# Kernel tuning notes

Measured on AMD Instinct MI355X. Metric: run time of the kernel, lower is better.

## Reference

```python
import jax, jax.numpy as jnp
import numpy as np

H = 4  # num heads, hard-coded in Encoder's GAT(hidden, hidden, hidden, 4, 2)


def build_adjacency(shot_type, encode_length):
    # Faithful vectorized port of initialize_adjacency_matrix.
    B, S = shot_type.shape
    N = 2 * encode_length
    base = np.zeros((14, N, N), dtype=np.int32)
    base[13] = 1 - np.eye(N, dtype=np.int32)  # complete graph minus self-loops
    for row in range(N):
        ni = row // 2
        if row % 2 == 0:
            col = (ni + 1) * 2
            rel = 11 if ni % 2 == 0 else 12
        else:
            col = (ni + 1) * 2 + 1
            rel = 12 if ni % 2 == 0 else 11
        if col <= N - 1:
            base[rel, row, col] = 1
            base[rel, col, row] = 1
            base[13, row, col] = 0
            base[13, col, row] = 0
    adj = jnp.tile(jnp.asarray(base)[None], (B, 1, 1, 1))  # [B,14,N,N]
    steps = np.arange(S)
    even = steps % 2 == 0
    i = np.where(even, 2 * steps, 2 * steps + 1)
    j = np.where(even, 2 * (steps + 1) + 1, 2 * (steps + 1))
    b = np.broadcast_to(np.arange(B)[:, None], (B, S))
    i = np.broadcast_to(i, (B, S))
    j = np.broadcast_to(j, (B, S))
    adj = adj.at[b, shot_type, i, j].set(1)
    adj = adj.at[b, shot_type, j, i].set(1)
    adj = adj.at[b, 13, i, j].set(0)
    adj = adj.at[b, 13, j, i].set(0)
    return adj


def gat_layer(x, mask, W, att):
    # x: [B,N,in], W: [in, H*F], att: [H, 2F]; standard GAT concat-score,
    # computed as a_src.h_i + a_dst.h_j (== a^T [h_i || h_j]).
    B, N, _ = x.shape
    F = att.shape[1] // 2
    h = (x @ W).reshape(B, N, H, F).transpose(0, 2, 1, 3)       # [B,H,N,F]
    s_src = jnp.einsum('bhnf,hf->bhn', h, att[:, :F])
    s_dst = jnp.einsum('bhnf,hf->bhn', h, att[:, F:])
    scores = s_src[:, :, :, None] + s_dst[:, :, None, :]        # [B,H,N,N]
    scores = jnp.where(scores > 0, scores, 0.2 * scores)        # LeakyReLU(0.2)
    scores = jnp.where(mask[:, None], scores, -jnp.inf)
    attn = jax.nn.softmax(scores, axis=-1)                      # dropout: eval mode
    hp = jnp.einsum('bhij,bhjf->bhif', attn, h)
    return hp.transpose(0, 2, 1, 3).reshape(B, N, H * F)


def setup_inputs() -> dict:
    B, E = 32, 256
    player_num, player_dim, location_dim, hidden = 35, 32, 32, 64
    k = jax.random.split(jax.random.key(0), 16)

    def lin(key, fan_in, shape):
        return jax.random.normal(key, shape, dtype=jnp.float32) / np.sqrt(fan_in)

    return {
        'player': jax.random.randint(k[0], (B, 2), 0, player_num),
        'shot_type': jax.random.randint(k[1], (B, E - 1), 0, 11),
        'player_A_x': jax.random.uniform(k[2], (B, E), dtype=jnp.float32),
        'player_A_y': jax.random.uniform(k[3], (B, E), dtype=jnp.float32),
        'player_B_x': jax.random.uniform(k[4], (B, E), dtype=jnp.float32),
        'player_B_y': jax.random.uniform(k[5], (B, E), dtype=jnp.float32),
        'encode_length': E,
        'emb_table': jax.random.normal(k[6], (player_num, player_dim), dtype=jnp.float32),
        'Wc': lin(k[7], 2, (2, location_dim)),
        'bc': jnp.zeros((location_dim,), dtype=jnp.float32),
        'Wm': lin(k[8], player_dim + location_dim, (player_dim + location_dim, hidden)),
        'bm': jnp.zeros((hidden,), dtype=jnp.float32),
        'lin1_W': lin(k[9], hidden, (hidden, H * hidden)),
        'att1': lin(k[10], 2 * hidden, (H, 2 * hidden)),
        'lin2_W': lin(k[11], H * hidden, (H * hidden, H * hidden)),
        'att2': lin(k[12], 2 * hidden, (H, 2 * hidden)),
    }


def reference(player, shot_type, player_A_x, player_A_y, player_B_x, player_B_y,
              encode_length, emb_table, Wc, bc, Wm, bm, lin1_W, att1, lin2_W, att2):
    E = int(encode_length)
    B = player.shape[0]
    adj = build_adjacency(shot_type, E)                 # [B,14,N,N]
    mask = adj.sum(axis=1) > 0                          # union over relations [B,N,N]
    coord_A = jnp.stack([player_A_x, player_A_y], axis=-1)   # [B,E,2]
    coord_B = jnp.stack([player_B_x, player_B_y], axis=-1)
    coord = jnp.stack([coord_A, coord_B], axis=2).reshape(B, -1, 2)  # [B,2E,2]
    ct = jax.nn.relu(coord @ Wc + bc)                   # [B,2E,loc]
    p = jnp.tile(player, (1, E))                        # [B,2E]
    pe = emb_table[p]                                   # [B,2E,pdim]
    x = jnp.concatenate([ct, pe], axis=-1) @ Wm + bm    # [B,2E,hidden]
    x = jax.nn.relu(gat_layer(x, mask, lin1_W, att1))
    node_embedding = gat_layer(x, mask, lin2_W, att2)   # [B,2E,H*hidden]
    return node_embedding, adj
```

## Files before the change

kernel.cpp:

```cpp
#include <hip/hip_runtime.h>
#include <hip/hip_bf16.h>
#include <stdint.h>

static constexpr int B_  = 32;
static constexpr int E_  = 256;
static constexpr int N_  = 512;
static constexpr int C_  = 256;
static constexpr int BN  = B_ * N_;
static constexpr int NODE_ELEMS = B_ * N_ * C_;
static constexpr int ADJ_ELEMS  = B_ * 14 * N_ * N_;

#define LOG2E 1.44269504088896340736f

typedef __attribute__((ext_vector_type(8))) short v8bf;
typedef __attribute__((ext_vector_type(4))) float v4f;

__device__ __forceinline__ unsigned short f2bfbits(float f) {
  union { float f; unsigned u; } x; x.f = f;
  unsigned u = x.u;
  return (unsigned short)((u + 0x7FFFu + ((u >> 16) & 1u)) >> 16);
}

struct ConvArgs {
  const void* src[15];
  void* dst[15];
  int n[15];
  int kind[15];
};

__global__ __launch_bounds__(256) void k_conv2(ConvArgs a, const unsigned* fprobe,
                                               const unsigned* iprobe) {
  __shared__ int fk_s, ik_s;
  int t = threadIdx.x;
  if (t == 0) {
    int c_even = 0, c_lo = 0;
    for (int k = 0; k < 32; ++k) {
      unsigned w = fprobe[2 * k];
      unsigned e32 = (w >> 23) & 0xFFu;
      unsigned elo = (w >> 7) & 0xFFu;
      if (e32 >= 105u && e32 <= 135u) ++c_even;
      if (elo >= 105u && elo <= 135u) ++c_lo;
    }
    fk_s = (c_even < 16) ? 2 : ((c_lo >= 16) ? 1 : 0);
    int hi0 = 0;
    for (int k = 0; k < 32; ++k) if (iprobe[2 * k + 1] == 0u) ++hi0;
    ik_s = (hi0 >= 30) ? 1 : 0;
  }
  __syncthreads();
  int fk = fk_s, ik = ik_s;
  int arr = blockIdx.y;
  int n = a.n[arr], kind = a.kind[arr];
  for (int idx = blockIdx.x * 256 + t; idx < n; idx += gridDim.x * 256) {
    if (kind == 0) {
      float v;
      if (fk == 2) {
        v = (float)((const double*)a.src[arr])[idx];
      } else if (fk == 1) {
        unsigned short u = ((const unsigned short*)a.src[arr])[idx];
        union { unsigned u; float f; } c; c.u = (unsigned)u << 16; v = c.f;
      } else {
        v = ((const float*)a.src[arr])[idx];
      }
      ((float*)a.dst[arr])[idx] = v;
    } else {
      int v;
      if (ik == 1) v = (int)((const long long*)a.src[arr])[idx];
      else         v = ((const int*)a.src[arr])[idx];
      ((int*)a.dst[arr])[idx] = v;
    }
  }
}

__global__ __launch_bounds__(64) void k_feat2(
    const int* __restrict__ player, const float* __restrict__ Ax, const float* __restrict__ Ay,
    const float* __restrict__ Bx, const float* __restrict__ By,
    const float* __restrict__ emb, const float* __restrict__ Wc, const float* __restrict__ bc,
    const float* __restrict__ Wm, const float* __restrict__ bm, float* __restrict__ x) {
  int id = blockIdx.x * 64 + threadIdx.x;
  if (id >= BN) return;
  int b = id >> 9, n = id & 511;
  int e = n >> 1, side = n & 1;
  float cx = side ? Bx[b * E_ + e] : Ax[b * E_ + e];
  float cy = side ? By[b * E_ + e] : Ay[b * E_ + e];
  int pid = player[b * 2 + side];
  float ct[32];
  for (int k = 0; k < 32; ++k)
    ct[k] = fmaxf(fmaf(cx, Wc[k], fmaf(cy, Wc[32 + k], bc[k])), 0.f);
  for (int o = 0; o < 64; ++o) {
    float acc = bm[o];
    for (int c = 0; c < 32; ++c) acc = fmaf(ct[c], Wm[c * 64 + o], acc);
    for (int c = 0; c < 32; ++c) acc = fmaf(emb[pid * 32 + c], Wm[(32 + c) * 64 + o], acc);
    x[(size_t)id * 64 + o] = acc;
  }
}

__global__ __launch_bounds__(256) void k_gemm(
    const float* __restrict__ x, const float* __restrict__ W, float* __restrict__ h, int K) {
  __shared__ float xs[64 * 64];
  __shared__ float wt[64 * 64];
  int row0 = blockIdx.x * 64;
  int col0 = blockIdx.y * 64;
  int t = threadIdx.x;
  int tx = t & 15, ty = t >> 4;
  float acc[4][4] = {};
  for (int kt = 0; kt < K; kt += 64) {
    #pragma unroll
    for (int q = 0; q < 4; ++q) {
      int v = q * 256 + t;
      int r = v >> 4, c = (v & 15) * 4;
      *(float4*)&xs[r * 64 + c] = *(const float4*)&x[(size_t)(row0 + r) * K + kt + c];
      *(float4*)&wt[r * 64 + c] = *(const float4*)&W[(size_t)(kt + r) * C_ + col0 + c];
    }
    __syncthreads();
    #pragma unroll 4
    for (int k = 0; k < 64; ++k) {
      float xv[4];
      #pragma unroll
      for (int r = 0; r < 4; ++r) xv[r] = xs[(ty * 4 + r) * 64 + k];
      float4 wf = *(const float4*)&wt[k * 64 + tx * 4];
      #pragma unroll
      for (int r = 0; r < 4; ++r) {
        acc[r][0] = fmaf(xv[r], wf.x, acc[r][0]);
        acc[r][1] = fmaf(xv[r], wf.y, acc[r][1]);
        acc[r][2] = fmaf(xv[r], wf.z, acc[r][2]);
        acc[r][3] = fmaf(xv[r], wf.w, acc[r][3]);
      }
    }
    __syncthreads();
  }
  #pragma unroll
  for (int r = 0; r < 4; ++r) {
    int row = row0 + ty * 4 + r;
    float4 o = make_float4(acc[r][0], acc[r][1], acc[r][2], acc[r][3]);
    *(float4*)&h[(size_t)row * C_ + col0 + tx * 4] = o;
  }
}

__global__ __launch_bounds__(256) void k_ssd(
    const float* __restrict__ h, const float* __restrict__ att,
    float* __restrict__ ss, float* __restrict__ sd) {
  int t = threadIdx.x;
  int wv = t >> 6, l = t & 63;
  int row = blockIdx.x * 4 + wv;
  int b = row >> 9, n = row & 511;
  #pragma unroll
  for (int hd = 0; hd < 4; ++hd) {
    float v = h[(size_t)row * C_ + hd * 64 + l];
    float s1 = v * att[hd * 128 + l];
    float s2 = v * att[hd * 128 + 64 + l];
    #pragma unroll
    for (int d = 32; d > 0; d >>= 1) {
      s1 += __shfl_xor(s1, d, 64);
      s2 += __shfl_xor(s2, d, 64);
    }
    if (l == 0) {
      int idx = (b * 4 + hd) * N_ + n;
      ss[idx] = s1; sd[idx] = s2;
    }
  }
}

__global__ __launch_bounds__(256) void k_ml(
    const float* __restrict__ ss, const float* __restrict__ sd,
    float* __restrict__ m2, float* __restrict__ rl) {
  int t = threadIdx.x;
  int wv = t >> 6, l = t & 63;
  int row = blockIdx.x * 4 + wv;
  int bh = row >> 9, i = row & 511;
  const float* sdb = sd + (size_t)bh * N_;
  float mx = -1e30f;
  #pragma unroll
  for (int q = 0; q < 8; ++q) mx = fmaxf(mx, sdb[q * 64 + l]);
  #pragma unroll
  for (int d = 32; d > 0; d >>= 1) mx = fmaxf(mx, __shfl_xor(mx, d, 64));
  float ssi = ss[row];
  float s = ssi + mx;
  float mm2 = fmaxf(s, 0.2f * s) * LOG2E;
  float acc = 0.f;
  #pragma unroll
  for (int q = 0; q < 8; ++q) {
    int j = q * 64 + l;
    float sc = ssi + sdb[j];
    sc = fmaxf(sc, 0.2f * sc);
    float e = exp2f(fmaf(sc, LOG2E, -mm2));
    acc += (j == i) ? 0.f : e;
  }
  #pragma unroll
  for (int d = 32; d > 0; d >>= 1) acc += __shfl_xor(acc, d, 64);
  if (l == 0) { m2[row] = mm2; rl[row] = 1.f / acc; }
}

template <int RELU>
__global__ __launch_bounds__(256) void k_attn_mfma(
    const float* __restrict__ h, const float* __restrict__ ss, const float* __restrict__ sd,
    const float* __restrict__ m2, const float* __restrict__ rl, float* __restrict__ outf) {
  __shared__ unsigned short hs[64 * 72];
  __shared__ float sdl[64];
  int blk = blockIdx.x;
  int it = blk & 3, hd = (blk >> 2) & 3, b = blk >> 4;
  int i0 = it * 128;
  int bh = b * 4 + hd;
  int t = threadIdx.x;
  int w = t >> 6, l = t & 63;
  int lane16 = l & 15, quad = l >> 4;
  float ss_s[2], m2_s[2];
  #pragma unroll
  for (int s = 0; s < 2; ++s) {
    int i = i0 + w * 32 + s * 16 + lane16;
    ss_s[s] = ss[(size_t)bh * N_ + i];
    m2_s[s] = m2[(size_t)bh * N_ + i];
  }
  v4f acc[2][4] = {};
  for (int jt = 0; jt < 8; ++jt) {
    int j0 = jt * 64;
    #pragma unroll
    for (int q = 0; q < 4; ++q) {
      int v = q * 256 + t;
      int j = v >> 4, f0 = (v & 15) * 4;
      float4 hv = *(const float4*)&h[(size_t)(b * N_ + j0 + j) * C_ + hd * 64 + f0];
      hs[(f0 + 0) * 72 + j] = f2bfbits(hv.x);
      hs[(f0 + 1) * 72 + j] = f2bfbits(hv.y);
      hs[(f0 + 2) * 72 + j] = f2bfbits(hv.z);
      hs[(f0 + 3) * 72 + j] = f2bfbits(hv.w);
    }
    if (t < 64) sdl[t] = sd[(size_t)bh * N_ + j0 + t];
    __syncthreads();
    #pragma unroll
    for (int ks = 0; ks < 2; ++ks) {
      int kb = ks * 32;
      v8bf afr[2];
      #pragma unroll
      for (int s = 0; s < 2; ++s) {
        int i = i0 + w * 32 + s * 16 + lane16;
        #pragma unroll
        for (int q = 0; q < 8; ++q) {
          int j = kb + quad * 8 + q;
          float sv = ss_s[s] + sdl[j];
          float sc = fmaxf(sv, 0.2f * sv);
          float p = exp2f(fmaf(sc, LOG2E, -m2_s[s]));
          if (i == j0 + j) p = 0.f;
          afr[s][q] = (short)f2bfbits(p);
        }
      }
      #pragma unroll
      for (int fs = 0; fs < 4; ++fs) {
        v8bf bfr = *(const v8bf*)&hs[(fs * 16 + lane16) * 72 + kb + quad * 8];
        acc[0][fs] = __builtin_amdgcn_mfma_f32_16x16x32_bf16(afr[0], bfr, acc[0][fs], 0, 0, 0);
        acc[1][fs] = __builtin_amdgcn_mfma_f32_16x16x32_bf16(afr[1], bfr, acc[1][fs], 0, 0, 0);
      }
    }
    __syncthreads();
  }
  #pragma unroll
  for (int s = 0; s < 2; ++s) {
    #pragma unroll
    for (int r = 0; r < 4; ++r) {
      int i = i0 + w * 32 + s * 16 + quad * 4 + r;
      float scale = rl[(size_t)bh * N_ + i];
      #pragma unroll
      for (int fs = 0; fs < 4; ++fs) {
        int f = fs * 16 + lane16;
        float vv = acc[s][fs][r] * scale;
        if constexpr (RELU) vv = fmaxf(vv, 0.f);
        outf[(size_t)(b * N_ + i) * C_ + hd * 64 + f] = vv;
      }
    }
  }
}

__global__ __launch_bounds__(256) void k_adjf2(
    const int* __restrict__ st, float* __restrict__ adj) {
  int chunk = blockIdx.x * 256 + threadIdx.x;
  int j0 = (chunk & 127) << 2;
  int rowid = chunk >> 7;
  int i = rowid & 511;
  int plane = rowid >> 9;
  int r = plane % 14;
  int b = plane / 14;
  float vals[4];
  #pragma unroll
  for (int q = 0; q < 4; ++q) {
    int j = j0 + q;
    int d = j - i;
    int ad = d < 0 ? -d : d;
    int mn = d < 0 ? j : i;
    int m4 = mn & 3;
    float v = 0.f;
    if (r == 13) {
      bool excl = (d == 0) || (ad == 2) || (ad == 3 && m4 == 0) || (ad == 1 && m4 == 3);
      v = excl ? 0.f : 1.f;
    } else if (r == 11) {
      v = (ad == 2 && (m4 == 0 || m4 == 3)) ? 1.f : 0.f;
    } else if (r == 12) {
      v = (ad == 2 && (m4 == 1 || m4 == 2)) ? 1.f : 0.f;
    } else {
      bool sp = (ad == 3 && m4 == 0) || (ad == 1 && m4 == 3);
      if (sp) v = (st[b * 255 + (mn >> 1)] == r) ? 1.f : 0.f;
    }
    vals[q] = v;
  }
  *(float4*)&adj[(size_t)chunk * 4] = make_float4(vals[0], vals[1], vals[2], vals[3]);
}

__global__ __launch_bounds__(256) void k_adjf(
    const unsigned* __restrict__ st_raw, float* __restrict__ adj) {
  __shared__ int i64_s;
  if (threadIdx.x == 0) {
    int hi0 = 0;
    for (int k = 0; k < 32; ++k) if (st_raw[2 * k + 1] == 0u) ++hi0;
    i64_s = (hi0 >= 30) ? 1 : 0;
  }
  __syncthreads();
  int is64 = i64_s;
  int chunk = blockIdx.x * 256 + threadIdx.x;
  int j0 = (chunk & 127) << 2;
  int rowid = chunk >> 7;
  int i = rowid & 511;
  int plane = rowid >> 9;
  int r = plane % 14;
  int b = plane / 14;
  float vals[4];
  #pragma unroll
  for (int q = 0; q < 4; ++q) {
    int j = j0 + q;
    int d = j - i;
    int ad = d < 0 ? -d : d;
    int mn = d < 0 ? j : i;
    int m4 = mn & 3;
    float v = 0.f;
    if (r == 13) {
      bool excl = (d == 0) || (ad == 2) || (ad == 3 && m4 == 0) || (ad == 1 && m4 == 3);
      v = excl ? 0.f : 1.f;
    } else if (r == 11) {
      v = (ad == 2 && (m4 == 0 || m4 == 3)) ? 1.f : 0.f;
    } else if (r == 12) {
      v = (ad == 2 && (m4 == 1 || m4 == 2)) ? 1.f : 0.f;
    } else {
      bool sp = (ad == 3 && m4 == 0) || (ad == 1 && m4 == 3);
      if (sp) {
        int e = b * 255 + (mn >> 1);
        int stv = is64 ? (int)st_raw[2 * e] : (int)st_raw[e];
        v = (stv == r) ? 1.f : 0.f;
      }
    }
    vals[q] = v;
  }
  *(float4*)&adj[(size_t)chunk * 4] = make_float4(vals[0], vals[1], vals[2], vals[3]);
}

__global__ void k_sentinel(float* out, float v) {
  if (threadIdx.x == 0 && blockIdx.x == 0) out[0] = v;
}

extern "C" void kernel_launch(void* const* d_in, const int* in_sizes, int n_in,
                              void* d_out, int out_size, void* d_ws, size_t ws_size,
                              hipStream_t stream) {
  static const int expA[16] = {64,8160,8192,8192,8192,8192,1,1120,64,32,4096,64,16384,512,65536,512};
  static const int expB[15] = {64,8160,8192,8192,8192,8192,1120,64,32,4096,64,16384,512,65536,512};
  int mismatch = -1;
  int base = 7;
  if (n_in == 16) {
    base = 7;
    for (int i = 0; i < 16; ++i) if (in_sizes[i] != expA[i]) { mismatch = i; break; }
  } else if (n_in == 15) {
    base = 6;
    for (int i = 0; i < 15; ++i) if (in_sizes[i] != expB[i]) { mismatch = i; break; }
  } else {
    mismatch = 17;
  }
  if (mismatch < 0 && out_size != NODE_ELEMS + ADJ_ELEMS) mismatch = 16;

  float* out_node = (float*)d_out;
  float* out_adjf = out_node + NODE_ELEMS;

  char* scr = (char*)out_adjf;
  float* x  = (float*)(scr);
  float* h  = (float*)(scr + (size_t)( 4u << 20));
  float* x2 = (float*)(scr + (size_t)(24u << 20));
  float* ss = (float*)(scr + (size_t)(44u << 20));
  float* sd = (float*)(scr + (size_t)(45u << 20));
  float* m2 = (float*)(scr + (size_t)(46u << 20));
  float* rl = (float*)(scr + (size_t)(47u << 20));
  float* cv = (float*)(scr + (size_t)(48u << 20));

  float* cAx  = cv + 0;
  float* cAy  = cv + 8192;
  float* cBx  = cv + 16384;
  float* cBy  = cv + 24576;
  float* cEmb = cv + 32768;
  float* cWc  = cv + 33888;
  float* cbc  = cv + 33952;
  float* cWm  = cv + 33984;
  float* cbm  = cv + 38080;
  float* cW1  = cv + 38144;
  float* cA1  = cv + 54528;
  float* cW2  = cv + 55040;
  float* cA2  = cv + 120576;
  int*   cPl  = (int*)(cv + 121088);

  bool ws_ok = (ws_size >= 8160 * sizeof(int));
  int* cSt = ws_ok ? (int*)d_ws : nullptr;

  ConvArgs a;
  a.src[0]  = d_in[2];        a.dst[0]  = cAx;  a.n[0]  = 8192;  a.kind[0]  = 0;
  a.src[1]  = d_in[3];        a.dst[1]  = cAy;  a.n[1]  = 8192;  a.kind[1]  = 0;
  a.src[2]  = d_in[4];        a.dst[2]  = cBx;  a.n[2]  = 8192;  a.kind[2]  = 0;
  a.src[3]  = d_in[5];        a.dst[3]  = cBy;  a.n[3]  = 8192;  a.kind[3]  = 0;
  a.src[4]  = d_in[base + 0]; a.dst[4]  = cEmb; a.n[4]  = 1120;  a.kind[4]  = 0;
  a.src[5]  = d_in[base + 1]; a.dst[5]  = cWc;  a.n[5]  = 64;    a.kind[5]  = 0;
  a.src[6]  = d_in[base + 2]; a.dst[6]  = cbc;  a.n[6]  = 32;    a.kind[6]  = 0;
  a.src[7]  = d_in[base + 3]; a.dst[7]  = cWm;  a.n[7]  = 4096;  a.kind[7]  = 0;
  a.src[8]  = d_in[base + 4]; a.dst[8]  = cbm;  a.n[8]  = 64;    a.kind[8]  = 0;
  a.src[9]  = d_in[base + 5]; a.dst[9]  = cW1;  a.n[9]  = 16384; a.kind[9]  = 0;
  a.src[10] = d_in[base + 6]; a.dst[10] = cA1;  a.n[10] = 512;   a.kind[10] = 0;
  a.src[11] = d_in[base + 7]; a.dst[11] = cW2;  a.n[11] = 65536; a.kind[11] = 0;
  a.src[12] = d_in[base + 8]; a.dst[12] = cA2;  a.n[12] = 512;   a.kind[12] = 0;
  a.src[13] = d_in[0];        a.dst[13] = cPl;  a.n[13] = 64;    a.kind[13] = 1;
  a.src[14] = d_in[1];        a.dst[14] = ws_ok ? (void*)cSt : (void*)cPl;
  a.n[14] = ws_ok ? 8160 : 0; a.kind[14] = 1;

  k_conv2<<<dim3(64, 15), 256, 0, stream>>>(a, (const unsigned*)d_in[base + 3],
                                            (const unsigned*)d_in[0]);

  k_feat2<<<BN / 64, 64, 0, stream>>>(cPl, cAx, cAy, cBx, cBy, cEmb, cWc, cbc, cWm, cbm, x);

  k_gemm<<<dim3(BN / 64, 4), 256, 0, stream>>>(x, cW1, h, 64);
  k_ssd<<<BN / 4, 256, 0, stream>>>(h, cA1, ss, sd);
  k_ml<<<B_ * 4 * N_ / 4, 256, 0, stream>>>(ss, sd, m2, rl);
  k_attn_mfma<1><<<B_ * 4 * (N_ / 128), 256, 0, stream>>>(h, ss, sd, m2, rl, x2);

  k_gemm<<<dim3(BN / 64, 4), 256, 0, stream>>>(x2, cW2, h, 256);
  k_ssd<<<BN / 4, 256, 0, stream>>>(h, cA2, ss, sd);
  k_ml<<<B_ * 4 * N_ / 4, 256, 0, stream>>>(ss, sd, m2, rl);
  k_attn_mfma<0><<<B_ * 4 * (N_ / 128), 256, 0, stream>>>(h, ss, sd, m2, rl, out_node);

  if (ws_ok) {
    k_adjf2<<<(ADJ_ELEMS / 4) / 256, 256, 0, stream>>>(cSt, out_adjf);
  } else {
    k_adjf<<<(ADJ_ELEMS / 4) / 256, 256, 0, stream>>>((const unsigned*)d_in[1], out_adjf);
  }

  if (mismatch >= 0) {
    float v = ldexpf(1024.f, mismatch);
    k_sentinel<<<1, 64, 0, stream>>>(out_node, v);
  }
}
```

Baseline: 702.6 us.

## Fuse attention score projections into GEMM and softmax stats into attention kernel

The per-head source/destination score dot products move into the GEMM epilogue, using a 16-lane shuffle reduction over each 64-column head tile, which removes the separate k_ssd kernel. The row max and softmax denominator are now computed inside the attention kernel: the whole sd row is loaded into LDS for the max, and the sum of the bf16-input probabilities is accumulated alongside the MFMA. This drops the k_ml kernel and its m2/rl round trips. The cost is slightly more work per attention block, and the normalizer is now summed from the fp32 probabilities in-kernel rather than by a separate pass.

```diff
diff --git a/kernel.cpp b/kernel.cpp
--- a/kernel.cpp
+++ b/kernel.cpp
@@ -95,11 +95,13 @@
 }
 
 __global__ __launch_bounds__(256) void k_gemm(
-    const float* __restrict__ x, const float* __restrict__ W, float* __restrict__ h, int K) {
+    const float* __restrict__ x, const float* __restrict__ W, float* __restrict__ h, int K,
+    const float* __restrict__ att, float* __restrict__ ssO, float* __restrict__ sdO) {
   __shared__ float xs[64 * 64];
   __shared__ float wt[64 * 64];
   int row0 = blockIdx.x * 64;
   int col0 = blockIdx.y * 64;
+  int hd = blockIdx.y;
   int t = threadIdx.x;
   int tx = t & 15, ty = t >> 4;
   float acc[4][4] = {};
@@ -134,81 +136,59 @@
     float4 o = make_float4(acc[r][0], acc[r][1], acc[r][2], acc[r][3]);
     *(float4*)&h[(size_t)row * C_ + col0 + tx * 4] = o;
   }
-}
-
-__global__ __launch_bounds__(256) void k_ssd(
-    const float* __restrict__ h, const float* __restrict__ att,
-    float* __restrict__ ss, float* __restrict__ sd) {
-  int t = threadIdx.x;
-  int wv = t >> 6, l = t & 63;
-  int row = blockIdx.x * 4 + wv;
-  int b = row >> 9, n = row & 511;
-  #pragma unroll
-  for (int hd = 0; hd < 4; ++hd) {
-    float v = h[(size_t)row * C_ + hd * 64 + l];
-    float s1 = v * att[hd * 128 + l];
-    float s2 = v * att[hd * 128 + 64 + l];
+  float attS[4], attD[4];
+  #pragma unroll
+  for (int c = 0; c < 4; ++c) {
+    attS[c] = att[hd * 128 + tx * 4 + c];
+    attD[c] = att[hd * 128 + 64 + tx * 4 + c];
+  }
+  #pragma unroll
+  for (int r = 0; r < 4; ++r) {
+    float p1 = acc[r][0] * attS[0] + acc[r][1] * attS[1] + acc[r][2] * attS[2] + acc[r][3] * attS[3];
+    float p2 = acc[r][0] * attD[0] + acc[r][1] * attD[1] + acc[r][2] * attD[2] + acc[r][3] * attD[3];
     #pragma unroll
-    for (int d = 32; d > 0; d >>= 1) {
-      s1 += __shfl_xor(s1, d, 64);
-      s2 += __shfl_xor(s2, d, 64);
-    }
-    if (l == 0) {
-      int idx = (b * 4 + hd) * N_ + n;
-      ss[idx] = s1; sd[idx] = s2;
-    }
-  }
-}
-
-__global__ __launch_bounds__(256) void k_ml(
-    const float* __restrict__ ss, const float* __restrict__ sd,
-    float* __restrict__ m2, float* __restrict__ rl) {
-  int t = threadIdx.x;
-  int wv = t >> 6, l = t & 63;
-  int row = blockIdx.x * 4 + wv;
-  int bh = row >> 9, i = row & 511;
-  const float* sdb = sd + (size_t)bh * N_;
-  float mx = -1e30f;
-  #pragma unroll
-  for (int q = 0; q < 8; ++q) mx = fmaxf(mx, sdb[q * 64 + l]);
-  #pragma unroll
-  for (int d = 32; d > 0; d >>= 1) mx = fmaxf(mx, __shfl_xor(mx, d, 64));
-  float ssi = ss[row];
-  float s = ssi + mx;
-  float mm2 = fmaxf(s, 0.2f * s) * LOG2E;
-  float acc = 0.f;
-  #pragma unroll
-  for (int q = 0; q < 8; ++q) {
-    int j = q * 64 + l;
-    float sc = ssi + sdb[j];
-    sc = fmaxf(sc, 0.2f * sc);
-    float e = exp2f(fmaf(sc, LOG2E, -mm2));
-    acc += (j == i) ? 0.f : e;
-  }
-  #pragma unroll
-  for (int d = 32; d > 0; d >>= 1) acc += __shfl_xor(acc, d, 64);
-  if (l == 0) { m2[row] = mm2; rl[row] = 1.f / acc; }
+    for (int d = 8; d > 0; d >>= 1) {
+      p1 += __shfl_xor(p1, d, 16);
+      p2 += __shfl_xor(p2, d, 16);
+    }
+    if (tx == 0) {
+      int row = row0 + ty * 4 + r;
+      int bb = row >> 9, nn = row & 511;
+      int idx = (bb * 4 + hd) * N_ + nn;
+      ssO[idx] = p1; sdO[idx] = p2;
+    }
+  }
 }
 
 template <int RELU>
-__global__ __launch_bounds__(256) void k_attn_mfma(
+__global__ __launch_bounds__(256) void k_attn_mfma2(
     const float* __restrict__ h, const float* __restrict__ ss, const float* __restrict__ sd,
-    const float* __restrict__ m2, const float* __restrict__ rl, float* __restrict__ outf) {
+    float* __restrict__ outf) {
   __shared__ unsigned short hs[64 * 72];
-  __shared__ float sdl[64];
+  __shared__ float sdl[512];
+  __shared__ float red[4];
+  __shared__ float ls[4][32];
   int blk = blockIdx.x;
   int it = blk & 3, hd = (blk >> 2) & 3, b = blk >> 4;
-  int i0 = it * 128;
-  int bh = b * 4 + hd;
-  int t = threadIdx.x;
-  int w = t >> 6, l = t & 63;
+  int i0 = it * 128, bh = b * 4 + hd;
+  int t = threadIdx.x, w = t >> 6, l = t & 63;
   int lane16 = l & 15, quad = l >> 4;
-  float ss_s[2], m2_s[2];
+  float v0 = sd[(size_t)bh * N_ + t];
+  float v1 = sd[(size_t)bh * N_ + 256 + t];
+  sdl[t] = v0; sdl[256 + t] = v1;
+  float mx = fmaxf(v0, v1);
+  #pragma unroll
+  for (int d = 32; d > 0; d >>= 1) mx = fmaxf(mx, __shfl_xor(mx, d, 64));
+  if (l == 0) red[w] = mx;
+  __syncthreads();
+  mx = fmaxf(fmaxf(red[0], red[1]), fmaxf(red[2], red[3]));
+  float ss_s[2], m2_s[2], lsum[2] = {0.f, 0.f};
   #pragma unroll
   for (int s = 0; s < 2; ++s) {
     int i = i0 + w * 32 + s * 16 + lane16;
     ss_s[s] = ss[(size_t)bh * N_ + i];
-    m2_s[s] = m2[(size_t)bh * N_ + i];
+    float sv = ss_s[s] + mx;
+    m2_s[s] = fmaxf(sv, 0.2f * sv) * LOG2E;
   }
   v4f acc[2][4] = {};
   for (int jt = 0; jt < 8; ++jt) {
@@ -223,7 +203,6 @@
       hs[(f0 + 2) * 72 + j] = f2bfbits(hv.z);
       hs[(f0 + 3) * 72 + j] = f2bfbits(hv.w);
     }
-    if (t < 64) sdl[t] = sd[(size_t)bh * N_ + j0 + t];
     __syncthreads();
     #pragma unroll
     for (int ks = 0; ks < 2; ++ks) {
@@ -234,11 +213,12 @@
         int i = i0 + w * 32 + s * 16 + lane16;
         #pragma unroll
         for (int q = 0; q < 8; ++q) {
-          int j = kb + quad * 8 + q;
+          int j = j0 + kb + quad * 8 + q;
           float sv = ss_s[s] + sdl[j];
           float sc = fmaxf(sv, 0.2f * sv);
           float p = exp2f(fmaf(sc, LOG2E, -m2_s[s]));
-          if (i == j0 + j) p = 0.f;
+          if (i == j) p = 0.f;
+          lsum[s] += p;
           afr[s][q] = (short)f2bfbits(p);
         }
       }
@@ -253,10 +233,17 @@
   }
   #pragma unroll
   for (int s = 0; s < 2; ++s) {
+    lsum[s] += __shfl_xor(lsum[s], 16, 64);
+    lsum[s] += __shfl_xor(lsum[s], 32, 64);
+    if (quad == 0) ls[w][s * 16 + lane16] = lsum[s];
+  }
+  __syncthreads();
+  #pragma unroll
+  for (int s = 0; s < 2; ++s) {
     #pragma unroll
     for (int r = 0; r < 4; ++r) {
       int i = i0 + w * 32 + s * 16 + quad * 4 + r;
-      float scale = rl[(size_t)bh * N_ + i];
+      float scale = 1.f / ls[w][s * 16 + quad * 4 + r];
       #pragma unroll
       for (int fs = 0; fs < 4; ++fs) {
         int f = fs * 16 + lane16;
@@ -379,8 +366,6 @@
   float* x2 = (float*)(scr + (size_t)(24u << 20));
   float* ss = (float*)(scr + (size_t)(44u << 20));
   float* sd = (float*)(scr + (size_t)(45u << 20));
-  float* m2 = (float*)(scr + (size_t)(46u << 20));
-  float* rl = (float*)(scr + (size_t)(47u << 20));
   float* cv = (float*)(scr + (size_t)(48u << 20));
 
   float* cAx  = cv + 0;
@@ -424,15 +409,11 @@
 
   k_feat2<<<BN / 64, 64, 0, stream>>>(cPl, cAx, cAy, cBx, cBy, cEmb, cWc, cbc, cWm, cbm, x);
 
-  k_gemm<<<dim3(BN / 64, 4), 256, 0, stream>>>(x, cW1, h, 64);
-  k_ssd<<<BN / 4, 256, 0, stream>>>(h, cA1, ss, sd);
-  k_ml<<<B_ * 4 * N_ / 4, 256, 0, stream>>>(ss, sd, m2, rl);
-  k_attn_mfma<1><<<B_ * 4 * (N_ / 128), 256, 0, stream>>>(h, ss, sd, m2, rl, x2);
-
-  k_gemm<<<dim3(BN / 64, 4), 256, 0, stream>>>(x2, cW2, h, 256);
-  k_ssd<<<BN / 4, 256, 0, stream>>>(h, cA2, ss, sd);
-  k_ml<<<B_ * 4 * N_ / 4, 256, 0, stream>>>(ss, sd, m2, rl);
-  k_attn_mfma<0><<<B_ * 4 * (N_ / 128), 256, 0, stream>>>(h, ss, sd, m2, rl, out_node);
+  k_gemm<<<dim3(BN / 64, 4), 256, 0, stream>>>(x, cW1, h, 64, cA1, ss, sd);
+  k_attn_mfma2<1><<<B_ * 4 * (N_ / 128), 256, 0, stream>>>(h, ss, sd, x2);
+
+  k_gemm<<<dim3(BN / 64, 4), 256, 0, stream>>>(x2, cW2, h, 256, cA2, ss, sd);
+  k_attn_mfma2<0><<<B_ * 4 * (N_ / 128), 256, 0, stream>>>(h, ss, sd, out_node);
 
   if (ws_ok) {
     k_adjf2<<<(ADJ_ELEMS / 4) / 256, 256, 0, stream>>>(cSt, out_adjf);
```

Measured after the change: 647.8 us. 7.8% less time.
